# Kernel tuning notes

Hardware: AMD Instinct MI355X
Metric: run time of the kernel (lower is better)

The kernel has to match this reference:

```python
import jax, jax.numpy as jnp
import numpy as np

VOC, EDIM, HDIM, SSZ, SDIM, SDEPTH, PAD = 32000, 256, 256, 128, 128, 2, 0
N, BSZ = 64, 32
T = 2 * N - 1  # 127
N_ACTS = 2  # push, pop


def _linear(key, out_d, in_d):
    k1, k2 = jax.random.split(key)
    return (jax.random.normal(k1, (out_d, in_d), jnp.float32) * 0.02,
            jax.random.normal(k2, (out_d,), jnp.float32) * 0.02)


def setup_inputs() -> dict:
    key = jax.random.key(0)
    ks = jax.random.split(key, 9)
    emb_W = jax.random.normal(ks[0], (VOC, EDIM), jnp.float32) * 0.02
    emb_W = emb_W.at[PAD].set(0.0)  # padding_idx row is zero in torch
    W_e2h, b_e2h = _linear(ks[1], HDIM, EDIM)
    W_s2h, b_s2h = _linear(ks[2], HDIM, SDIM * SDEPTH)
    W_h2h, b_h2h = _linear(ks[3], HDIM, HDIM)
    W_h2i, b_h2i = _linear(ks[4], N_ACTS + 1, HDIM)
    W_h2s, b_h2s = _linear(ks[5], SDIM, HDIM)
    W_s2u, b_s2u = _linear(ks[6], SDIM, SDIM * SDEPTH)
    empty_elem = jax.random.normal(ks[7], (1, SDIM), jnp.float32) * 0.02
    inputs = jax.random.randint(ks[8], (N, BSZ), 0, VOC)
    return dict(inputs=inputs, emb_W=emb_W, W_e2h=W_e2h, b_e2h=b_e2h,
                W_s2h=W_s2h, b_s2h=b_s2h, W_h2h=W_h2h, b_h2h=b_h2h,
                W_h2i=W_h2i, b_h2i=b_h2i, W_h2s=W_h2s, b_h2s=b_h2s,
                W_s2u=W_s2u, b_s2u=b_s2u, empty_elem=empty_elem)


def _srnn(inputs, emb_W, W_e2h, b_e2h, W_s2h, b_s2h, W_h2h, b_h2h,
          W_h2i, b_h2i, W_h2s, b_h2s, W_s2u, b_s2u, empty_elem):
    bsz = inputs.shape[1]
    embs = emb_W[inputs]                                        # [N, bsz, edim]
    pads = jnp.broadcast_to(emb_W[PAD], (T - N, bsz, EDIM))     # padded tail
    buf0 = jnp.concatenate([embs, pads], axis=0)                # [T, bsz, edim]
    hid0 = jnp.zeros((bsz, HDIM), jnp.float32)
    stack0 = jnp.broadcast_to(empty_elem, (bsz, SSZ, SDIM))

    def step(carry, t):
        hid, stack, buf = carry
        tops = stack[:, :SDEPTH, :].reshape(bsz, SDEPTH * SDIM)
        inp = buf[t]                                            # [bsz, edim]
        ihid = inp @ W_e2h.T + b_e2h + tops @ W_s2h.T + b_s2h
        hid = jax.nn.relu(hid @ W_h2h.T + b_h2h + ihid)
        inst = ihid @ W_h2i.T + b_h2i                           # [bsz, 3]
        act = jax.nn.softmax(inst[:, :N_ACTS], axis=-1)
        gamma = 1.0 + jnp.log1p(jnp.exp(inst[:, N_ACTS:]))      # [bsz, 1]
        a = act ** gamma
        a = a / (jnp.sum(a, axis=-1, keepdims=True) + 1e-16)    # sharpened acts
        p_push, p_pop = a[:, :1], a[:, 1:]                      # [bsz, 1]
        # buffer update: pop shifts the whole buffer down one slot along time
        buf_pop = jnp.concatenate([jnp.zeros_like(buf[:1]), buf[:-1]], axis=0)
        buf = p_push[None] * buf + p_pop[None] * buf_pop        # [1,bsz,1] bcast
        push_val = jax.nn.relu(hid @ W_h2s.T + b_h2s)           # [bsz, sdim]
        u_val = jax.nn.relu(tops @ W_s2u.T + b_s2u)             # [bsz, sdim]
        z = jnp.zeros((bsz, 1, SDIM), jnp.float32)
        # W_push (shift down by 1) as an index roll
        stack_push = jnp.concatenate([z, stack[:, :-1, :]], axis=1)
        stack_push = stack_push.at[:, 0, :].add(push_val)
        # W_pop = shift up by SDEPTH, then W_push = shift down by 1
        up = jnp.concatenate([stack[:, SDEPTH:, :],
                              jnp.zeros((bsz, SDEPTH, SDIM), jnp.float32)], axis=1)
        stack_pop = jnp.concatenate([z, up[:, :-1, :]], axis=1)
        stack_pop = stack_pop.at[:, 0, :].add(u_val)
        stack_pop = stack_pop.at[:, SSZ - SDEPTH + 1:, :].add(empty_elem[0])
        stack = p_push[:, :, None] * stack_push + p_pop[:, :, None] * stack_pop
        return (hid, stack, buf), (hid, a, stack[:, 0, :])

    (hid, stack, _), (outputs, acts, top_elems) = jax.lax.scan(
        step, (hid0, stack0, buf0), jnp.arange(T))
    return outputs, hid, stack, acts, top_elems


def reference(inputs, emb_W, W_e2h, b_e2h, W_s2h, b_s2h, W_h2h, b_h2h,
              W_h2i, b_h2i, W_h2s, b_h2s, W_s2u, b_s2u, empty_elem):
    return _srnn(inputs, emb_W, W_e2h, b_e2h, W_s2h, b_s2h, W_h2h, b_h2h,
                 W_h2i, b_h2i, W_h2s, b_h2s, W_s2u, b_s2u, empty_elem)
```

## Files before the change

### kernel.cpp

```cpp
#include <hip/hip_runtime.h>
#include <stdint.h>
#include <math.h>


#define T_STEPS 127

#define OUT_OFF   0
#define HID_OFF   1040384
#define STACK_OFF 1048576
#define ACTS_OFF  1572864
#define TE_OFF    1580992

#define WB_OFF 16384
#define E2H_OFF_U 131072

typedef _Float16 h2 __attribute__((ext_vector_type(2)));

__device__ __forceinline__ unsigned packh2(float a, float b){
  h2 v; v.x = (_Float16)a; v.y = (_Float16)b;
  return __builtin_bit_cast(unsigned, v);
}
__device__ __forceinline__ float h2loF(unsigned u){ h2 v = __builtin_bit_cast(h2,u); return (float)v.x; }
__device__ __forceinline__ float h2hiF(unsigned u){ h2 v = __builtin_bit_cast(h2,u); return (float)v.y; }

#if __has_builtin(__builtin_amdgcn_fdot2)
__device__ __forceinline__ float fdot2(unsigned a, unsigned b, float c){
  return __builtin_amdgcn_fdot2(__builtin_bit_cast(h2,a), __builtin_bit_cast(h2,b), c, false);
}
#else
__device__ __forceinline__ float fdot2(unsigned a, unsigned b, float c){
  return c + h2loF(a)*h2loF(b) + h2hiF(a)*h2hiF(b);
}
#endif

#if __has_builtin(__builtin_amdgcn_exp2f)
#define EXP2F(x) __builtin_amdgcn_exp2f(x)
#else
#define EXP2F(x) exp2f(x)
#endif
#if __has_builtin(__builtin_amdgcn_logf)
#define LOG2F(x) __builtin_amdgcn_logf(x)
#else
#define LOG2F(x) log2f(x)
#endif
#if __has_builtin(__builtin_amdgcn_rcpf)
#define RCPF(x) __builtin_amdgcn_rcpf(x)
#else
#define RCPF(x) (1.f/(x))
#endif

#define BAR() asm volatile("s_waitcnt lgkmcnt(0)\n\ts_barrier" ::: "memory")

#define CHOFF(u) (12*((u)>>3) + ((u)&7))

__global__ void prep_pack(const float* __restrict__ We2h, const float* __restrict__ Ws2h,
                          const float* __restrict__ Wh2h, const float* __restrict__ Wh2s,
                          const float* __restrict__ Ws2u, uint4* __restrict__ out4){
  int gid = blockIdx.x*256 + threadIdx.x;
  const float* src;
  if (gid < 16384){
    int i = gid >> 10, t_ = gid & 1023;
    const float* S = (t_ < 512) ? Ws2h : Wh2h;
    int r = t_ & 511, jp = r >> 2, ks = r & 3;
    int j = 2*jp + (i >> 3);
    int k0 = ks*64 + (i & 7)*8;
    src = S + j*256 + k0;
  } else if (gid < 24576){
    int l = gid - 16384;
    int i = l >> 10, t_ = l & 1023;
    const float* S = (t_ < 512) ? Wh2s : Ws2u;
    int tt = t_ & 511;
    int j  = 2*(tt >> 3) + (i >> 2);
    int k0 = (tt & 7)*32 + (i & 3)*8;
    src = S + j*256 + k0;
  } else {
    int l = gid - 24576;
    int i8 = l >> 8, j = l & 255;
    src = We2h + j*256 + i8*8;
  }
  uint4 r4;
  r4.x = packh2(src[0], src[1]); r4.y = packh2(src[2], src[3]);
  r4.z = packh2(src[4], src[5]); r4.w = packh2(src[6], src[7]);
  out4[gid] = r4;
}

__global__ void prep_e2h(const int* __restrict__ inputs, const float* __restrict__ embW,
                         const uint4* __restrict__ w04, unsigned* __restrict__ e2hpk){
  __shared__ float emb[8][256];
  int tid = threadIdx.x;
  int r2 = blockIdx.x >> 3, bg = blockIdx.x & 7;
  for (int q=0;q<8;q++){
    int rr = q >> 2, bb = q & 3;
    int tok = inputs[(2*r2+rr)*32 + bg*4+bb];
    emb[q][tid] = embW[tok*256 + tid];
  }
  __syncthreads();
  float acc[8] = {0.f,0.f,0.f,0.f,0.f,0.f,0.f,0.f};
  for (int i8=0;i8<32;i8++){
    uint4 u = w04[i8*256 + tid];
    unsigned uu[4] = {u.x,u.y,u.z,u.w};
    #pragma unroll
    for (int c=0;c<4;c++){
      float lo = h2loF(uu[c]), hi = h2hiF(uu[c]);
      int k = i8*8 + c*2;
      #pragma unroll
      for (int q=0;q<8;q++)
        acc[q] += emb[q][k]*lo + emb[q][k+1]*hi;
    }
  }
  int base = (bg*4)*8192 + r2*256 + tid;
  #pragma unroll
  for (int bb=0;bb<4;bb++)
    e2hpk[base + bb*8192] = packh2(acc[bb], acc[4+bb]);
}

__global__ __attribute__((amdgpu_flat_work_group_size(1024,1024), amdgpu_waves_per_eu(4,4)))
void srnn_main(const uint4* __restrict__ ws4, const unsigned* __restrict__ wsu,
               const float* __restrict__ b_e2h, const float* __restrict__ b_s2h,
               const float* __restrict__ b_h2h, const float* __restrict__ Wh2i,
               const float* __restrict__ b_h2i, const float* __restrict__ b_h2s,
               const float* __restrict__ b_s2u, const float* __restrict__ empty_el,
               float* __restrict__ out)
{
  __shared__ __align__(16) float    stk_s[128*128];
  __shared__ __align__(16) unsigned e2h_s[32*258];
  __shared__ __align__(16) float    halo_top[2][16*128];
  __shared__ __align__(16) float    halo_bot[2][16*128];
  __shared__ __align__(16) unsigned s_pk[192];
  __shared__ __align__(16) unsigned hid_pk[192];
  __shared__ __align__(16) float    pv_s[128], uv_s[128];
  __shared__ __align__(16) float    accih[256], acchp[256];
  __shared__ __align__(16) float    emptyf_s[128];
  __shared__ __align__(16) float    whi_s[768];
  __shared__ __align__(16) float    wbuf[2][192];
  __shared__ __align__(16) unsigned pkwc[32];
  __shared__ float    pp_s, pq_s;

  const int tid = threadIdx.x;
  const int b   = blockIdx.x;
  const int aside = tid >> 9;
  const int ar  = tid & 511;
  const int ajp = ar >> 2;
  const int aks = ar & 3;
  const int pB  = tid >> 3;
  const int kB  = tid & 7;
  const int g   = tid >> 6;
  const int cp  = tid & 63;
  const int sub = (tid >> 5) & 1;
  const int c4  = tid & 31;

  uint4 w1r[16], wBr[8];
  #pragma unroll
  for (int i=0;i<16;i++) w1r[i] = ws4[i*1024 + tid];
  #pragma unroll
  for (int i=0;i<8;i++)  wBr[i] = ws4[WB_OFF + i*1024 + tid];

  float bA0=0.f, bA1=0.f;
  if (aks==0){
    int j0 = 2*ajp;
    if (aside==0){ bA0 = b_e2h[j0]+b_s2h[j0]; bA1 = b_e2h[j0+1]+b_s2h[j0+1]; }
    else         { bA0 = b_h2h[j0];           bA1 = b_h2h[j0+1]; }
  }
  float bB0=0.f, bB1=0.f;
  if (kB==0){
    if (pB < 64){ bB0 = b_h2s[2*pB];      bB1 = b_h2s[2*pB+1]; }
    else        { bB0 = b_s2u[2*(pB-64)]; bB1 = b_s2u[2*(pB-64)+1]; }
  }
  const float bi0=b_h2i[0], bi1=b_h2i[1], bi2=b_h2i[2];

  const unsigned* e2hg = wsu + E2H_OFF_U + b*8192;
  #pragma unroll
  for (int q=0;q<8;q++){
    int idx = q*1024 + tid;
    e2h_s[(idx>>8)*258 + (idx&255)] = e2hg[idx];
  }
  {
    float2 e2 = *(const float2*)&empty_el[2*cp];
    #pragma unroll
    for (int j=0;j<8;j++)
      *(float2*)&stk_s[(8*g+j)*128 + 2*cp] = e2;
    *(float2*)&halo_top[0][g*128 + 2*cp] = e2;
    *(float2*)&halo_bot[0][g*128 + 2*cp] = e2;
  }
  if (tid < 128){
    emptyf_s[tid] = empty_el[tid];
    hid_pk[CHOFF(tid)] = 0u;
    int cu = tid & 63;
    s_pk[CHOFF(tid)] = packh2(empty_el[2*cu], empty_el[2*cu+1]);
  }
  if (tid < 768) whi_s[tid] = Wh2i[tid];
  if (tid < 192){ wbuf[0][tid] = (tid==64)?1.f:0.f; wbuf[1][tid]=0.f; }
  if (tid < 32)  pkwc[tid] = (tid==0)? packh2(1.f,0.f) : 0u;
  __syncthreads();

  int cur = 0;
  for (int t=0;t<T_STEPS;++t){
    {
      const unsigned* act  = aside ? hid_pk : s_pk;
      const unsigned* actB = act + 48*aks;
      float x0 = 0.f, x1 = 0.f;
      if (aside==0){
        uint4 cwa = *(const uint4*)&pkwc[8*aks];
        uint4 cwb = *(const uint4*)&pkwc[8*aks+4];
        unsigned cwv[8] = {cwa.x,cwa.y,cwa.z,cwa.w,cwb.x,cwb.y,cwb.z,cwb.w};
        #pragma unroll
        for (int q=0;q<8;q++){
          int r2 = aks*8 + q;
          unsigned cw = cwv[q];
          uint2 e = *(const uint2*)&e2h_s[r2*258 + 2*ajp];
          x0 = fdot2(cw, e.x, x0);
          x1 = fdot2(cw, e.y, x1);
        }
      }
      #pragma unroll
      for (int i=0;i<8;i++){
        uint4 A  = *(const uint4*)(actB + 12*(i>>1) + 4*(i&1));
        uint4 Wa = w1r[i], Wb = w1r[8+i];
        x0 = fdot2(A.x,Wa.x,x0); x0 = fdot2(A.y,Wa.y,x0);
        x0 = fdot2(A.z,Wa.z,x0); x0 = fdot2(A.w,Wa.w,x0);
        x1 = fdot2(A.x,Wb.x,x1); x1 = fdot2(A.y,Wb.y,x1);
        x1 = fdot2(A.z,Wb.z,x1); x1 = fdot2(A.w,Wb.w,x1);
      }
      x0 += __shfl_xor(x0,1); x0 += __shfl_xor(x0,2);
      x1 += __shfl_xor(x1,1); x1 += __shfl_xor(x1,2);
      if (aks==0){
        float* dst = aside ? acchp : accih;
        *(float2*)&dst[2*ajp] = make_float2(x0 + bA0, x1 + bA1);
      }
    }
    BAR();

    if (tid < 64){
      float4 av = *(const float4*)&accih[4*tid];
      float4 q0 = *(const float4*)&whi_s[      4*tid];
      float4 q1 = *(const float4*)&whi_s[256 + 4*tid];
      float4 q2 = *(const float4*)&whi_s[512 + 4*tid];
      float p0 = av.x*q0.x + av.y*q0.y + av.z*q0.z + av.w*q0.w;
      float p1 = av.x*q1.x + av.y*q1.y + av.z*q1.z + av.w*q1.w;
      float p2 = av.x*q2.x + av.y*q2.y + av.z*q2.z + av.w*q2.w;
      #pragma unroll
      for (int o=1;o<=32;o<<=1){
        p0 += __shfl_xor(p0,o); p1 += __shfl_xor(p1,o); p2 += __shfl_xor(p2,o);
      }
      if (tid==0){
        float i0 = bi0+p0, i1 = bi1+p1, gi = bi2+p2;
        float gamma = 1.f + 0.6931471806f*LOG2F(1.f + EXP2F(1.442695041f*gi));
        float z = 1.442695041f*gamma*(i0 - i1);
        float ppv = RCPF(1.f + EXP2F(-z));
        float pqv = 1.f - ppv;
        pp_s = ppv; pq_s = pqv;
        *(float2*)&out[ACTS_OFF + t*64 + b*2] = make_float2(ppv,pqv);
      }
    }
    if (tid >= 64 && tid < 192){
      int hl = tid - 64;
      float2 ih2 = *(const float2*)&accih[2*hl];
      float2 hp2 = *(const float2*)&acchp[2*hl];
      float hn0 = fmaxf(ih2.x+hp2.x, 0.f);
      float hn1 = fmaxf(ih2.y+hp2.y, 0.f);
      hid_pk[CHOFF(hl)] = packh2(hn0,hn1);
      *(float2*)&out[OUT_OFF + t*8192 + b*256 + 2*hl] = make_float2(hn0,hn1);
      if (t==T_STEPS-1) *(float2*)&out[HID_OFF + b*256 + 2*hl] = make_float2(hn0,hn1);
    }
    BAR();

    {
      const unsigned* srcB = (pB < 64) ? hid_pk : s_pk;
      const uint4* cA0 = (const uint4*)(srcB + 24*kB);
      const uint4* cA1 = (const uint4*)(srcB + 24*kB + 12);
      uint4 A0 = cA0[0], A1 = cA0[1];
      uint4 A2 = cA1[0], A3 = cA1[1];
      float y0=0.f, y1=0.f;
      y0=fdot2(A0.x,wBr[0].x,y0); y0=fdot2(A0.y,wBr[0].y,y0); y0=fdot2(A0.z,wBr[0].z,y0); y0=fdot2(A0.w,wBr[0].w,y0);
      y0=fdot2(A1.x,wBr[1].x,y0); y0=fdot2(A1.y,wBr[1].y,y0); y0=fdot2(A1.z,wBr[1].z,y0); y0=fdot2(A1.w,wBr[1].w,y0);
      y0=fdot2(A2.x,wBr[2].x,y0); y0=fdot2(A2.y,wBr[2].y,y0); y0=fdot2(A2.z,wBr[2].z,y0); y0=fdot2(A2.w,wBr[2].w,y0);
      y0=fdot2(A3.x,wBr[3].x,y0); y0=fdot2(A3.y,wBr[3].y,y0); y0=fdot2(A3.z,wBr[3].z,y0); y0=fdot2(A3.w,wBr[3].w,y0);
      y1=fdot2(A0.x,wBr[4].x,y1); y1=fdot2(A0.y,wBr[4].y,y1); y1=fdot2(A0.z,wBr[4].z,y1); y1=fdot2(A0.w,wBr[4].w,y1);
      y1=fdot2(A1.x,wBr[5].x,y1); y1=fdot2(A1.y,wBr[5].y,y1); y1=fdot2(A1.z,wBr[5].z,y1); y1=fdot2(A1.w,wBr[5].w,y1);
      y1=fdot2(A2.x,wBr[6].x,y1); y1=fdot2(A2.y,wBr[6].y,y1); y1=fdot2(A2.z,wBr[6].z,y1); y1=fdot2(A2.w,wBr[6].w,y1);
      y1=fdot2(A3.x,wBr[7].x,y1); y1=fdot2(A3.y,wBr[7].y,y1); y1=fdot2(A3.z,wBr[7].z,y1); y1=fdot2(A3.w,wBr[7].w,y1);
      y0 += __shfl_xor(y0,1); y0 += __shfl_xor(y0,2); y0 += __shfl_xor(y0,4);
      y1 += __shfl_xor(y1,1); y1 += __shfl_xor(y1,2); y1 += __shfl_xor(y1,4);
      if (kB==0){
        float v0 = fmaxf(y0+bB0,0.f), v1 = fmaxf(y1+bB1,0.f);
        if (pB < 64) *(float2*)&pv_s[2*pB]      = make_float2(v0,v1);
        else         *(float2*)&uv_s[2*(pB-64)] = make_float2(v0,v1);
      }
    }
    BAR();
    const float pp = pp_s, pq = pq_s;

    {
      const int R = 8*g + 4*sub;
      float4 o0, o1, o2, o3, o4, o5;
      o1 = *(const float4*)&stk_s[(R  )*128 + 4*c4];
      o2 = *(const float4*)&stk_s[(R+1)*128 + 4*c4];
      o3 = *(const float4*)&stk_s[(R+2)*128 + 4*c4];
      o4 = *(const float4*)&stk_s[(R+3)*128 + 4*c4];
      if (sub == 0){
        o0 = (g>0) ? *(const float4*)&halo_bot[cur][(g-1)*128 + 4*c4]
                   : make_float4(0.f,0.f,0.f,0.f);
        o5 = *(const float4*)&stk_s[(R+4)*128 + 4*c4];
      } else {
        o0 = *(const float4*)&stk_s[(R-1)*128 + 4*c4];
        o5 = (g<15) ? *(const float4*)&halo_top[cur][(g+1)*128 + 4*c4]
                    : *(const float4*)&emptyf_s[4*c4];
      }
      float4 n0, n1, n2, n3;
      n0.x = pp*o0.x + pq*o2.x; n0.y = pp*o0.y + pq*o2.y;
      n0.z = pp*o0.z + pq*o2.z; n0.w = pp*o0.w + pq*o2.w;
      n1.x = pp*o1.x + pq*o3.x; n1.y = pp*o1.y + pq*o3.y;
      n1.z = pp*o1.z + pq*o3.z; n1.w = pp*o1.w + pq*o3.w;
      n2.x = pp*o2.x + pq*o4.x; n2.y = pp*o2.y + pq*o4.y;
      n2.z = pp*o2.z + pq*o4.z; n2.w = pp*o2.w + pq*o4.w;
      n3.x = pp*o3.x + pq*o5.x; n3.y = pp*o3.y + pq*o5.y;
      n3.z = pp*o3.z + pq*o5.z; n3.w = pp*o3.w + pq*o5.w;
      if (g == 0 && sub == 0){
        float4 pv4 = *(const float4*)&pv_s[4*c4];
        float4 uv4 = *(const float4*)&uv_s[4*c4];
        n0.x = pp*pv4.x + pq*uv4.x; n0.y = pp*pv4.y + pq*uv4.y;
        n0.z = pp*pv4.z + pq*uv4.z; n0.w = pp*pv4.w + pq*uv4.w;
      }
      *(float4*)&stk_s[(R  )*128 + 4*c4] = n0;
      *(float4*)&stk_s[(R+1)*128 + 4*c4] = n1;
      *(float4*)&stk_s[(R+2)*128 + 4*c4] = n2;
      *(float4*)&stk_s[(R+3)*128 + 4*c4] = n3;
      if (sub == 0) *(float4*)&halo_top[cur^1][g*128 + 4*c4] = n0;
      else          *(float4*)&halo_bot[cur^1][g*128 + 4*c4] = n3;
      if (g == 0 && sub == 0){
        *(float4*)&out[TE_OFF + t*4096 + b*128 + 4*c4] = n0;
        s_pk[CHOFF(2*c4)]      = packh2(n0.x, n0.y);
        s_pk[CHOFF(2*c4+1)]    = packh2(n0.z, n0.w);
        s_pk[CHOFF(64+2*c4)]   = packh2(n1.x, n1.y);
        s_pk[CHOFF(64+2*c4+1)] = packh2(n1.z, n1.w);
      }
      if (tid < 128){
        int k = 64+tid;
        wbuf[cur^1][k] = pp*wbuf[cur][k] + pq*wbuf[cur][k-1];
      } else if (tid < 160){
        int r2 = tid-128;
        int k1 = 65 + t - 2*r2;
        float wa = wbuf[cur][k1], wb2 = wbuf[cur][k1-1], wc2 = wbuf[cur][k1-2];
        pkwc[r2] = packh2(pp*wa+pq*wb2, pp*wb2+pq*wc2);
      }
    }
    BAR();
    cur ^= 1;
  }

  {
    const int R = 8*g + 4*sub;
    #pragma unroll
    for (int j=0;j<4;j++){
      *(float4*)&out[STACK_OFF + b*16384 + (R+j)*128 + 4*c4] =
        *(const float4*)&stk_s[(R+j)*128 + 4*c4];
    }
  }
}

extern "C" void kernel_launch(void* const* d_in, const int* in_sizes, int n_in,
                              void* d_out, int out_size, void* d_ws, size_t ws_size,
                              hipStream_t stream){
  const int*   inputs = (const int*)d_in[0];
  const float* embW   = (const float*)d_in[1];
  const float* We2h   = (const float*)d_in[2];
  const float* b_e2h  = (const float*)d_in[3];
  const float* Ws2h   = (const float*)d_in[4];
  const float* b_s2h  = (const float*)d_in[5];
  const float* Wh2h   = (const float*)d_in[6];
  const float* b_h2h  = (const float*)d_in[7];
  const float* Wh2i   = (const float*)d_in[8];
  const float* b_h2i  = (const float*)d_in[9];
  const float* Wh2s   = (const float*)d_in[10];
  const float* b_h2s  = (const float*)d_in[11];
  const float* Ws2u   = (const float*)d_in[12];
  const float* b_s2u  = (const float*)d_in[13];
  const float* empty  = (const float*)d_in[14];
  unsigned* wsu = (unsigned*)d_ws;

  prep_pack<<<dim3(128), dim3(256), 0, stream>>>(We2h, Ws2h, Wh2h, Wh2s, Ws2u, (uint4*)wsu);
  prep_e2h<<<dim3(256), dim3(256), 0, stream>>>(inputs, embW, ((const uint4*)wsu)+24576, wsu + E2H_OFF_U);
  srnn_main<<<dim3(32), dim3(1024), 0, stream>>>((const uint4*)wsu, (const unsigned*)wsu,
                                                 b_e2h, b_s2h, b_h2h, Wh2i, b_h2i,
                                                 b_h2s, b_s2u, empty, (float*)d_out);
}
```

Baseline: 828.5 us.

## Overlap s2u GEMV with hidden update and use DPP lane reductions

Moves the stack-to-update GEMV, which depends only on the stack tops, into the same barrier phase as the action/hidden computation, carried out by the upper 512 threads. The barrier-separated phase then handles only the hidden-to-push GEMV, which removes serialized work from the per-step critical path. It also replaces ds_swizzle/bpermute shuffles with DPP row operations for the small butterfly reductions. The DPP row_half_mirror/row_mirror patterns are not true XORs, but summing over a symmetric group still gives the correct total. The change assumes pB>=64 exactly for tid>=512.

Result: faster. 756.4 us (-8.7%).

```diff
diff --git a/kernel.cpp b/kernel.cpp
--- a/kernel.cpp
+++ b/kernel.cpp
@@ -48,6 +48,16 @@
 #else
 #define RCPF(x) (1.f/(x))
 #endif
+
+#define DPP_XOR1 0xB1
+#define DPP_XOR2 0x4E
+#define DPP_HM   0x141
+#define DPP_RM   0x140
+template<int CTRL>
+__device__ __forceinline__ float dppadd(float v){
+  int s = __builtin_amdgcn_update_dpp(0, __builtin_bit_cast(int, v), CTRL, 0xF, 0xF, true);
+  return v + __builtin_bit_cast(float, s);
+}
 
 #define BAR() asm volatile("s_waitcnt lgkmcnt(0)\n\ts_barrier" ::: "memory")
 
@@ -114,6 +124,22 @@
     e2hpk[base + bb*8192] = packh2(acc[bb], acc[4+bb]);
 }
 
+#define GEMV_B(SRC, Y0, Y1) \
+  { const uint4* cA0_ = (const uint4*)((SRC) + 24*kB); \
+    uint4 A0_ = cA0_[0], A1_ = cA0_[1]; \
+    const uint4* cA1_ = (const uint4*)((SRC) + 24*kB + 12); \
+    uint4 A2_ = cA1_[0], A3_ = cA1_[1]; \
+    Y0=fdot2(A0_.x,wBr[0].x,Y0); Y0=fdot2(A0_.y,wBr[0].y,Y0); Y0=fdot2(A0_.z,wBr[0].z,Y0); Y0=fdot2(A0_.w,wBr[0].w,Y0); \
+    Y0=fdot2(A1_.x,wBr[1].x,Y0); Y0=fdot2(A1_.y,wBr[1].y,Y0); Y0=fdot2(A1_.z,wBr[1].z,Y0); Y0=fdot2(A1_.w,wBr[1].w,Y0); \
+    Y0=fdot2(A2_.x,wBr[2].x,Y0); Y0=fdot2(A2_.y,wBr[2].y,Y0); Y0=fdot2(A2_.z,wBr[2].z,Y0); Y0=fdot2(A2_.w,wBr[2].w,Y0); \
+    Y0=fdot2(A3_.x,wBr[3].x,Y0); Y0=fdot2(A3_.y,wBr[3].y,Y0); Y0=fdot2(A3_.z,wBr[3].z,Y0); Y0=fdot2(A3_.w,wBr[3].w,Y0); \
+    Y1=fdot2(A0_.x,wBr[4].x,Y1); Y1=fdot2(A0_.y,wBr[4].y,Y1); Y1=fdot2(A0_.z,wBr[4].z,Y1); Y1=fdot2(A0_.w,wBr[4].w,Y1); \
+    Y1=fdot2(A1_.x,wBr[5].x,Y1); Y1=fdot2(A1_.y,wBr[5].y,Y1); Y1=fdot2(A1_.z,wBr[5].z,Y1); Y1=fdot2(A1_.w,wBr[5].w,Y1); \
+    Y1=fdot2(A2_.x,wBr[6].x,Y1); Y1=fdot2(A2_.y,wBr[6].y,Y1); Y1=fdot2(A2_.z,wBr[6].z,Y1); Y1=fdot2(A2_.w,wBr[6].w,Y1); \
+    Y1=fdot2(A3_.x,wBr[7].x,Y1); Y1=fdot2(A3_.y,wBr[7].y,Y1); Y1=fdot2(A3_.z,wBr[7].z,Y1); Y1=fdot2(A3_.w,wBr[7].w,Y1); \
+    Y0 = dppadd<DPP_XOR1>(Y0); Y0 = dppadd<DPP_XOR2>(Y0); Y0 = dppadd<DPP_HM>(Y0); \
+    Y1 = dppadd<DPP_XOR1>(Y1); Y1 = dppadd<DPP_XOR2>(Y1); Y1 = dppadd<DPP_HM>(Y1); }
+
 __global__ __attribute__((amdgpu_flat_work_group_size(1024,1024), amdgpu_waves_per_eu(4,4)))
 void srnn_main(const uint4* __restrict__ ws4, const unsigned* __restrict__ wsu,
                const float* __restrict__ b_e2h, const float* __restrict__ b_s2h,
@@ -221,8 +247,8 @@
         x1 = fdot2(A.x,Wb.x,x1); x1 = fdot2(A.y,Wb.y,x1);
         x1 = fdot2(A.z,Wb.z,x1); x1 = fdot2(A.w,Wb.w,x1);
       }
-      x0 += __shfl_xor(x0,1); x0 += __shfl_xor(x0,2);
-      x1 += __shfl_xor(x1,1); x1 += __shfl_xor(x1,2);
+      x0 = dppadd<DPP_XOR1>(x0); x0 = dppadd<DPP_XOR2>(x0);
+      x1 = dppadd<DPP_XOR1>(x1); x1 = dppadd<DPP_XOR2>(x1);
       if (aks==0){
         float* dst = aside ? acchp : accih;
         *(float2*)&dst[2*ajp] = make_float2(x0 + bA0, x1 + bA1);
@@ -238,10 +264,15 @@
       float p0 = av.x*q0.x + av.y*q0.y + av.z*q0.z + av.w*q0.w;
       float p1 = av.x*q1.x + av.y*q1.y + av.z*q1.z + av.w*q1.w;
       float p2 = av.x*q2.x + av.y*q2.y + av.z*q2.z + av.w*q2.w;
-      #pragma unroll
-      for (int o=1;o<=32;o<<=1){
-        p0 += __shfl_xor(p0,o); p1 += __shfl_xor(p1,o); p2 += __shfl_xor(p2,o);
-      }
+      p0 = dppadd<DPP_XOR1>(p0); p0 = dppadd<DPP_XOR2>(p0);
+      p0 = dppadd<DPP_HM>(p0);   p0 = dppadd<DPP_RM>(p0);
+      p1 = dppadd<DPP_XOR1>(p1); p1 = dppadd<DPP_XOR2>(p1);
+      p1 = dppadd<DPP_HM>(p1);   p1 = dppadd<DPP_RM>(p1);
+      p2 = dppadd<DPP_XOR1>(p2); p2 = dppadd<DPP_XOR2>(p2);
+      p2 = dppadd<DPP_HM>(p2);   p2 = dppadd<DPP_RM>(p2);
+      p0 += __shfl_xor(p0,16); p0 += __shfl_xor(p0,32);
+      p1 += __shfl_xor(p1,16); p1 += __shfl_xor(p1,32);
+      p2 += __shfl_xor(p2,16); p2 += __shfl_xor(p2,32);
       if (tid==0){
         float i0 = bi0+p0, i1 = bi1+p1, gi = bi2+p2;
         float gamma = 1.f + 0.6931471806f*LOG2F(1.f + EXP2F(1.442695041f*gi));
@@ -251,8 +282,7 @@
         pp_s = ppv; pq_s = pqv;
         *(float2*)&out[ACTS_OFF + t*64 + b*2] = make_float2(ppv,pqv);
       }
-    }
-    if (tid >= 64 && tid < 192){
+    } else if (tid < 192){
       int hl = tid - 64;
       float2 ih2 = *(const float2*)&accih[2*hl];
       float2 hp2 = *(const float2*)&acchp[2*hl];
@@ -262,29 +292,22 @@
       *(float2*)&out[OUT_OFF + t*8192 + b*256 + 2*hl] = make_float2(hn0,hn1);
       if (t==T_STEPS-1) *(float2*)&out[HID_OFF + b*256 + 2*hl] = make_float2(hn0,hn1);
     }
+    if (tid >= 512){
+      float y0=0.f, y1=0.f;
+      GEMV_B(s_pk, y0, y1);
+      if (kB==0){
+        *(float2*)&uv_s[2*(pB-64)] =
+          make_float2(fmaxf(y0+bB0,0.f), fmaxf(y1+bB1,0.f));
+      }
+    }
     BAR();
 
-    {
-      const unsigned* srcB = (pB < 64) ? hid_pk : s_pk;
-      const uint4* cA0 = (const uint4*)(srcB + 24*kB);
-      const uint4* cA1 = (const uint4*)(srcB + 24*kB + 12);
-      uint4 A0 = cA0[0], A1 = cA0[1];
-      uint4 A2 = cA1[0], A3 = cA1[1];
+    if (tid < 512){
       float y0=0.f, y1=0.f;
-      y0=fdot2(A0.x,wBr[0].x,y0); y0=fdot2(A0.y,wBr[0].y,y0); y0=fdot2(A0.z,wBr[0].z,y0); y0=fdot2(A0.w,wBr[0].w,y0);
-      y0=fdot2(A1.x,wBr[1].x,y0); y0=fdot2(A1.y,wBr[1].y,y0); y0=fdot2(A1.z,wBr[1].z,y0); y0=fdot2(A1.w,wBr[1].w,y0);
-      y0=fdot2(A2.x,wBr[2].x,y0); y0=fdot2(A2.y,wBr[2].y,y0); y0=fdot2(A2.z,wBr[2].z,y0); y0=fdot2(A2.w,wBr[2].w,y0);
-      y0=fdot2(A3.x,wBr[3].x,y0); y0=fdot2(A3.y,wBr[3].y,y0); y0=fdot2(A3.z,wBr[3].z,y0); y0=fdot2(A3.w,wBr[3].w,y0);
-      y1=fdot2(A0.x,wBr[4].x,y1); y1=fdot2(A0.y,wBr[4].y,y1); y1=fdot2(A0.z,wBr[4].z,y1); y1=fdot2(A0.w,wBr[4].w,y1);
-      y1=fdot2(A1.x,wBr[5].x,y1); y1=fdot2(A1.y,wBr[5].y,y1); y1=fdot2(A1.z,wBr[5].z,y1); y1=fdot2(A1.w,wBr[5].w,y1);
-      y1=fdot2(A2.x,wBr[6].x,y1); y1=fdot2(A2.y,wBr[6].y,y1); y1=fdot2(A2.z,wBr[6].z,y1); y1=fdot2(A2.w,wBr[6].w,y1);
-      y1=fdot2(A3.x,wBr[7].x,y1); y1=fdot2(A3.y,wBr[7].y,y1); y1=fdot2(A3.z,wBr[7].z,y1); y1=fdot2(A3.w,wBr[7].w,y1);
-      y0 += __shfl_xor(y0,1); y0 += __shfl_xor(y0,2); y0 += __shfl_xor(y0,4);
-      y1 += __shfl_xor(y1,1); y1 += __shfl_xor(y1,2); y1 += __shfl_xor(y1,4);
+      GEMV_B(hid_pk, y0, y1);
       if (kB==0){
-        float v0 = fmaxf(y0+bB0,0.f), v1 = fmaxf(y1+bB1,0.f);
-        if (pB < 64) *(float2*)&pv_s[2*pB]      = make_float2(v0,v1);
-        else         *(float2*)&uv_s[2*(pB-64)] = make_float2(v0,v1);
+        *(float2*)&pv_s[2*pB] =
+          make_float2(fmaxf(y0+bB0,0.f), fmaxf(y1+bB1,0.f));
       }
     }
     BAR();
```
